# Performance work log

Measured on AMD Instinct MI355X. Metric: run time of the kernel, lower is better.

## Reference

```python
import jax, jax.numpy as jnp
from jax import lax
import numpy as np

LEAK = 0.95  # leaking_rate

SEQ, B, IN, H, OUT, L = 512, 32, 128, 2048, 128, 3


def setup_inputs() -> dict:
    key = jax.random.key(0)
    ks = jax.random.split(key, 12)
    in_scale = 1.0 / np.sqrt(IN)
    h_scale = 1.0 / np.sqrt(H)
    # spectral_radius=0.9: Gaussian NxN with std s has spectral radius ~ s*sqrt(N)
    rec_scale = 0.9 / np.sqrt(H)
    return {
        "input": jax.random.normal(ks[0], (SEQ, B, IN), jnp.float32),
        "w_ih0": jax.random.normal(ks[1], (H, IN), jnp.float32) * in_scale,
        "b_ih0": jax.random.normal(ks[2], (H,), jnp.float32) * 0.1,
        "w_hh0": jax.random.normal(ks[3], (H, H), jnp.float32) * rec_scale,
        "w_ih1": jax.random.normal(ks[4], (H, H), jnp.float32) * h_scale,
        "b_ih1": jax.random.normal(ks[5], (H,), jnp.float32) * 0.1,
        "w_hh1": jax.random.normal(ks[6], (H, H), jnp.float32) * rec_scale,
        "w_ih2": jax.random.normal(ks[7], (H, H), jnp.float32) * h_scale,
        "b_ih2": jax.random.normal(ks[8], (H,), jnp.float32) * 0.1,
        "w_hh2": jax.random.normal(ks[9], (H, H), jnp.float32) * rec_scale,
        "w_out": jax.random.normal(ks[10], (OUT, L * H), jnp.float32) * (1.0 / np.sqrt(L * H)),
        "b_out": jax.random.normal(ks[11], (OUT,), jnp.float32) * 0.1,
        "washout": 32,
    }


def reference(input, w_ih0, b_ih0, w_hh0, w_ih1, b_ih1, w_hh1,
              w_ih2, b_ih2, w_hh2, w_out, b_out, washout):
    a = jnp.asarray(LEAK, input.dtype)
    Bsz = input.shape[1]
    Hd = w_hh0.shape[0]

    def step(carry, x_t):
        h0, h1, h2 = carry
        # leaky-integrated tanh reservoir, layer-stacked (DeepESN)
        h0 = (1 - a) * h0 + a * jnp.tanh(x_t @ w_ih0.T + b_ih0 + h0 @ w_hh0.T)
        h1 = (1 - a) * h1 + a * jnp.tanh(h0 @ w_ih1.T + b_ih1 + h1 @ w_hh1.T)
        h2 = (1 - a) * h2 + a * jnp.tanh(h1 @ w_ih2.T + b_ih2 + h2 @ w_hh2.T)
        return (h0, h1, h2), jnp.concatenate([h0, h1, h2], axis=-1)

    init = tuple(jnp.zeros((Bsz, Hd), input.dtype) for _ in range(3))
    (h0, h1, h2), states = lax.scan(step, init, input)  # states: [S, B, L*H]
    states = states[washout:]                            # discard washout steps
    out = states @ w_out.T + b_out                       # [S-washout, B, OUT]
    hidden = jnp.stack([h0, h1, h2], axis=0)             # [L, B, H]
    return out, hidden
```

## Files before the change

### kernel.cpp

```cpp
#include <hip/hip_runtime.h>
#include <hip/hip_bf16.h>


typedef unsigned short u16;
typedef __attribute__((ext_vector_type(8))) __bf16 bf16x8;
typedef __attribute__((ext_vector_type(4))) float f32x4;

#define MFMA_AG(acc, a, w) \
  asm volatile("v_mfma_f32_16x16x32_bf16 %0, %1, %2, %0" : "+v"(acc) : "v"(a), "a"(w))

#define KC0 72
#define KC1 128
#define KCP 192
#define E0P (128*KC0*512)
#define E1P (128*KC1*512)
#define EPP (8*KCP*512)
#define CH 1024
#define S0 (68*CH)
#define S12 (64*CH)
#define NSLOT 8

static __device__ __forceinline__ float b2f(u16 u){ return __uint_as_float(((unsigned)u)<<16); }
static __device__ __forceinline__ u16 f2b(float f){ unsigned x=__float_as_uint(f); return (u16)((x + 0x7FFFu + ((x>>16)&1u))>>16); }
static __device__ __forceinline__ int frag_addr(int b, int j){
  int c=j>>5, ko=j&31, half=b>>4, lane=(b&15)|((ko>>3)<<4), e=ko&7;
  return ((c*2+half)*64+lane)*8+e;
}
static __device__ __forceinline__ bf16x8 asbf(f32x4 v){ union U{f32x4 f; bf16x8 b;} u; u.f=v; return u.b; }

static __device__ __forceinline__ f32x4 ld16_sc(const u16* p){
  f32x4 r;
  asm volatile("global_load_dwordx4 %0, %1, off sc0 sc1" : "=v"(r) : "v"(p));
  return r;
}
static __device__ __forceinline__ f32x4 ld16_pl(const float* p){
  f32x4 r;
  asm volatile("global_load_dwordx4 %0, %1, off" : "=v"(r) : "v"(p));
  return r;
}
static __device__ __forceinline__ void st_b128_sc(u16* p, f32x4 v){
  asm volatile("global_store_dwordx4 %0, %1, off sc0 sc1" :: "v"(p), "v"(v) : "memory");
}
static __device__ __forceinline__ void st_b32_sc(unsigned* p, unsigned v){
  asm volatile("global_store_dword %0, %1, off sc0 sc1" :: "v"(p), "v"(v) : "memory");
}
static __device__ __forceinline__ void drain(){
  asm volatile("s_waitcnt vmcnt(0)" ::: "memory");
}
#define WAITV(n) do{ asm volatile("s_waitcnt vmcnt(" #n ")" ::: "memory"); __builtin_amdgcn_sched_barrier(0); }while(0)

static __device__ __forceinline__ void poll4(int lane,
    const unsigned* a, unsigned ta,
    const unsigned* b, unsigned tb,
    const unsigned* c, unsigned tc, int nc,
    const unsigned* d, unsigned td)
{
  for(;;){
    unsigned va=0, vb=0, vc=0, vd=0;
    asm volatile("global_load_dword %0, %1, off sc0 sc1" : "=v"(va) : "v"(a+lane));
    if (b) asm volatile("global_load_dword %0, %1, off sc0 sc1" : "=v"(vb) : "v"(b+lane));
    if (c) asm volatile("global_load_dword %0, %1, off sc0 sc1" : "=v"(vc) : "v"(c+(lane<nc?lane:0)));
    if (d) asm volatile("global_load_dword %0, %1, off sc0 sc1" : "=v"(vd) : "v"(d+(lane<8?lane:0)));
    asm volatile("s_waitcnt vmcnt(0)" ::: "memory");
    __builtin_amdgcn_sched_barrier(0);
    bool ok = (va>=ta);
    if (b) ok &= (vb>=tb);
    if (c) ok &= (lane>=nc) || (vc>=tc);
    if (d) ok &= (lane>=8) || (vd>=td);
    if (__all(ok)) return;
    __builtin_amdgcn_s_sleep(1);
  }
}

__global__ __launch_bounds__(256) void k_pack(const float* __restrict__ wih0, const float* __restrict__ whh0,
    const float* __restrict__ wih1, const float* __restrict__ whh1,
    const float* __restrict__ wih2, const float* __restrict__ whh2,
    const float* __restrict__ wout,
    u16* __restrict__ p0, u16* __restrict__ p1, u16* __restrict__ p2, u16* __restrict__ po)
{
  const long SRC0 = 2048L*2176, SRC1 = 2048L*4096, SRCP = 128L*6144;
  const long total8 = (SRC0 + 2*SRC1 + SRCP) >> 3;
  for (long id = (long)blockIdx.x*blockDim.x + threadIdx.x; id < total8; id += (long)gridDim.x*blockDim.x){
    long r = id<<3; int KC, j, k; u16* dst;
    const float* sa; const float* sb; int split;
    if (r < SRC0){ KC=KC0; j=(int)(r/2176); k=(int)(r%2176); sa=wih0+(size_t)j*128; sb=whh0+(size_t)j*2048; split=128; dst=p0; }
    else if ((r -= SRC0) < SRC1){ KC=KC1; j=(int)(r/4096); k=(int)(r%4096); sa=wih1+(size_t)j*2048; sb=whh1+(size_t)j*2048; split=2048; dst=p1; }
    else if ((r -= SRC1) < SRC1){ KC=KC1; j=(int)(r/4096); k=(int)(r%4096); sa=wih2+(size_t)j*2048; sb=whh2+(size_t)j*2048; split=2048; dst=p2; }
    else { r -= SRC1; KC=KCP; j=(int)(r/6144); k=(int)(r%6144); sa=wout+(size_t)j*6144; sb=sa; split=6144; dst=po; }
    const float* src = (k<split) ? (sa + k) : (sb + (k - split));
    u16 tmp[8];
    #pragma unroll
    for (int e=0;e<8;e++) tmp[e] = f2b(src[e]);
    int jt=j>>4, jl=j&15, c=k>>5, ko=k&31, lane=((ko>>3)<<4)|jl;
    u16* dp = dst + (((size_t)jt*KC + c)*64 + lane)*8;
    *(f32x4*)dp = *(f32x4*)tmp;
  }
}

#define L12_ISS(s0, c0) \
  _Pragma("unroll") \
  for (int i=0;i<4;++i){ \
    sa[(s0)+i]=ld16_sc(apb + (size_t)((c0)+i)*CH); \
    sb[(s0)+i]=ld16_sc(apb + (size_t)((c0)+i)*CH + 512); \
  }
#define L12_MM(s0, c0) \
  _Pragma("unroll") \
  for (int i=0;i<4;++i){ \
    bf16x8 a0=asbf(sa[(s0)+i]), a1=asbf(sb[(s0)+i]); \
    MFMA_AG(acc00,a0,wreg[0][(c0)+i]); MFMA_AG(acc01,a1,wreg[0][(c0)+i]); \
    MFMA_AG(acc10,a0,wreg[1][(c0)+i]); MFMA_AG(acc11,a1,wreg[1][(c0)+i]); \
  }
#define PIN_ACC4() asm volatile("s_nop 1" : "+v"(acc00), "+v"(acc01), "+v"(acc10), "+v"(acc11))
#define FENCE_ACC4() asm volatile("s_nop 7\n\ts_nop 7" : "+v"(acc00), "+v"(acc01), "+v"(acc10), "+v"(acc11))

static __device__ __forceinline__ void run_l12(
    const u16* __restrict__ pW, const float* __restrict__ bias,
    const u16* __restrict__ A0slots, size_t a0stride, u16* OWN,
    unsigned* SEQup, unsigned* SEQown, unsigned* Sc, int nc, unsigned* Sd,
    int jt0, float (*red)[2][2][256], u16* ldsout)
{
  const int tid=threadIdx.x, w=tid>>6, ln=tid&63;
  bf16x8 wreg[2][16];
  #pragma unroll
  for (int u=0;u<2;u++)
    #pragma unroll
    for (int ci=0;ci<16;ci++)
      wreg[u][ci] = *(const bf16x8*)(pW + (((size_t)(jt0+u)*KC1 + (w*16+ci))*64 + ln)*8);

  const int h_=tid>>8, pos=tid&255, l_=pos>>2, i_=pos&3, col_=l_&15, row_=((l_>>4)<<2)+i_, b_=(h_<<4)+row_;
  const float bv0=bias[(jt0<<4)+col_], bv1=bias[((jt0+1)<<4)+col_];
  const int ko0=col_, ko1=16+col_;
  const int faw0=((h_*64)+((b_&15)|((ko0>>3)<<4)))*8+(ko0&7);
  const int faw1=((h_*64)+((b_&15)|((ko1>>3)<<4)))*8+(ko1&7);
  const int myc=jt0>>1, gidx=jt0>>1;

  if (tid<128) *(f32x4*)(ldsout+tid*8) = (f32x4){0,0,0,0};
  __syncthreads();

  for (int t=0;t<512;t++){
    if (tid<64){
      poll4(tid, SEQup,(unsigned)(t+1), SEQown,(unsigned)t,
            (t>=NSLOT)?Sc:nullptr,(unsigned)(t-7),nc,
            (t>=NSLOT)?Sd:nullptr,(unsigned)(t-7));
    }
    __syncthreads();
    const int cur=t&7, prv=(t+7)&7;
    const u16* a0base = (w<4) ? A0slots + (size_t)cur*a0stride + (size_t)(w*16)*CH
                              : OWN + (size_t)prv*S12 + (size_t)((w-4)*16)*CH;
    const u16* apb = a0base + (size_t)ln*8;
    f32x4 sa[8], sb[8];
    f32x4 acc00={0,0,0,0},acc01={0,0,0,0},acc10={0,0,0,0},acc11={0,0,0,0};
    PIN_ACC4();
    L12_ISS(0,0); L12_ISS(4,4);
    WAITV(8); L12_MM(0,0); L12_ISS(0,8);
    WAITV(8); L12_MM(4,4); L12_ISS(4,12);
    WAITV(8); L12_MM(0,8);
    WAITV(0); L12_MM(4,12);
    FENCE_ACC4();
    #pragma unroll
    for (int i=0;i<4;i++){
      red[w][0][0][(ln<<2)+i]=acc00[i]; red[w][0][1][(ln<<2)+i]=acc01[i];
      red[w][1][0][(ln<<2)+i]=acc10[i]; red[w][1][1][(ln<<2)+i]=acc11[i];
    }
    __syncthreads();
    {
      float v0=0.f, v1=0.f;
      #pragma unroll
      for (int ww=0;ww<8;ww++){ v0 += red[ww][0][h_][pos]; v1 += red[ww][1][h_][pos]; }
      float hp0 = b2f(ldsout[faw0]);
      float hp1 = b2f(ldsout[faw1]);
      ldsout[faw0] = f2b(0.05f*hp0 + 0.95f*tanhf(v0 + bv0));
      ldsout[faw1] = f2b(0.05f*hp1 + 0.95f*tanhf(v1 + bv1));
    }
    __syncthreads();
    if (tid<128){
      f32x4 vv = *(const f32x4*)(ldsout + tid*8);
      st_b128_sc(OWN + (size_t)cur*S12 + (size_t)myc*CH + tid*8, vv);
    }
    drain();
    __syncthreads();
    if (tid==0) st_b32_sc(SEQown+gidx, (unsigned)(t+1));
  }
}

#define X_ISSUE(ci) do{ \
    const float* q0 = xf + rr*128 + (ci)*32 + kg*8; \
    xs0[ci]=ld16_pl(q0); xs1[ci]=ld16_pl(q0+4); \
    xs2[ci]=ld16_pl(q0+2048); xs3[ci]=ld16_pl(q0+2052); \
  }while(0)
#define X_MFMA(ci) do{ \
    bf16x8 a0,a1; \
    _Pragma("unroll") \
    for (int e=0;e<4;e++){ a0[e]=(__bf16)xs0[ci][e]; a0[e+4]=(__bf16)xs1[ci][e]; \
                           a1[e]=(__bf16)xs2[ci][e]; a1[e+4]=(__bf16)xs3[ci][e]; } \
    asm volatile("s_nop 1" : "+v"(a0), "+v"(a1)); \
    MFMA_AG(acc00,a0,wreg[0][ci]); MFMA_AG(acc01,a1,wreg[0][ci]); \
    MFMA_AG(acc10,a0,wreg[1][ci]); MFMA_AG(acc11,a1,wreg[1][ci]); \
  }while(0)
#define LH_ISSUE(ci) do{ sa[ci]=ld16_sc(hbp + (size_t)(ci)*CH); sb[ci]=ld16_sc(hbp + (size_t)(ci)*CH + 512); }while(0)
#define LH_MFMA(ci) do{ \
    bf16x8 a0=asbf(sa[ci]), a1=asbf(sb[ci]); \
    MFMA_AG(acc00,a0,wreg[0][ci]); MFMA_AG(acc01,a1,wreg[0][ci]); \
    MFMA_AG(acc10,a0,wreg[1][ci]); MFMA_AG(acc11,a1,wreg[1][ci]); \
  }while(0)

static __device__ __forceinline__ void run_l0(
    const u16* __restrict__ pW, const float* __restrict__ bias, const float* __restrict__ input,
    u16* H0, unsigned* SEQ0, unsigned* SEQ1, unsigned* SEQ3,
    int jt0, float (*red)[2][2][256], u16* ldsout)
{
  const int tid=threadIdx.x, w=tid>>6, ln=tid&63, rr=ln&15, kg=ln>>4;
  bf16x8 wreg[2][9];
  #pragma unroll
  for (int u=0;u<2;u++)
    #pragma unroll
    for (int ci=0;ci<9;ci++)
      wreg[u][ci] = *(const bf16x8*)(pW + (((size_t)(jt0+u)*KC0 + (w*9+ci))*64 + ln)*8);

  const int h_=tid>>8, pos=tid&255, l_=pos>>2, i_=pos&3, col_=l_&15, row_=((l_>>4)<<2)+i_, b_=(h_<<4)+row_;
  const float bv0=bias[(jt0<<4)+col_], bv1=bias[((jt0+1)<<4)+col_];
  const int ko0=col_, ko1=16+col_;
  const int faw0=((h_*64)+((b_&15)|((ko0>>3)<<4)))*8+(ko0&7);
  const int faw1=((h_*64)+((b_&15)|((ko1>>3)<<4)))*8+(ko1&7);
  const int myc=jt0>>1, gidx=jt0>>1;

  if (tid<128) *(f32x4*)(ldsout+tid*8) = (f32x4){0,0,0,0};
  __syncthreads();

  for (int t=0;t<512;t++){
    if (tid<64){
      poll4(tid, SEQ0,(unsigned)t, (t>=NSLOT)?SEQ1:nullptr,(unsigned)(t-7),
            (t>=NSLOT)?SEQ3:nullptr,(unsigned)(t-7),8, nullptr,0u);
    }
    __syncthreads();
    const int cur=t&7, prv=(t+7)&7;
    const float* xf = input + (size_t)t*4096;
    const u16* h0prv = H0 + (size_t)prv*S0;
    f32x4 acc00={0,0,0,0},acc01={0,0,0,0},acc10={0,0,0,0},acc11={0,0,0,0};
    PIN_ACC4();
    if (w==0){
      f32x4 xs0[4],xs1[4],xs2[4],xs3[4], sa[9], sb[9];
      const u16* hbp = h0prv - (size_t)4*CH + (size_t)ln*8;
      X_ISSUE(0); X_ISSUE(1);
      X_ISSUE(2); X_ISSUE(3); WAITV(8); X_MFMA(0); X_MFMA(1);
      LH_ISSUE(4); LH_ISSUE(5); LH_ISSUE(6); LH_ISSUE(7); LH_ISSUE(8);
      WAITV(10); X_MFMA(2); X_MFMA(3);
      WAITV(0);
      LH_MFMA(4); LH_MFMA(5); LH_MFMA(6); LH_MFMA(7); LH_MFMA(8);
    } else {
      f32x4 sa[9], sb[9];
      const u16* hbp = h0prv + (size_t)(w*9-4)*CH + (size_t)ln*8;
      LH_ISSUE(0); LH_ISSUE(1); LH_ISSUE(2); LH_ISSUE(3);
      LH_ISSUE(4); LH_ISSUE(5); LH_ISSUE(6); LH_ISSUE(7);
      WAITV(8);  LH_MFMA(0); LH_MFMA(1); LH_MFMA(2); LH_MFMA(3);
      LH_ISSUE(8);
      WAITV(2);  LH_MFMA(4); LH_MFMA(5); LH_MFMA(6); LH_MFMA(7);
      WAITV(0);  LH_MFMA(8);
    }
    FENCE_ACC4();
    #pragma unroll
    for (int i=0;i<4;i++){
      red[w][0][0][(ln<<2)+i]=acc00[i]; red[w][0][1][(ln<<2)+i]=acc01[i];
      red[w][1][0][(ln<<2)+i]=acc10[i]; red[w][1][1][(ln<<2)+i]=acc11[i];
    }
    __syncthreads();
    {
      float v0=0.f, v1=0.f;
      #pragma unroll
      for (int ww=0;ww<8;ww++){ v0 += red[ww][0][h_][pos]; v1 += red[ww][1][h_][pos]; }
      float hp0 = b2f(ldsout[faw0]);
      float hp1 = b2f(ldsout[faw1]);
      ldsout[faw0] = f2b(0.05f*hp0 + 0.95f*tanhf(v0 + bv0));
      ldsout[faw1] = f2b(0.05f*hp1 + 0.95f*tanhf(v1 + bv1));
    }
    __syncthreads();
    if (tid<128){
      f32x4 vv = *(const f32x4*)(ldsout + tid*8);
      st_b128_sc(H0 + (size_t)cur*S0 + (size_t)myc*CH + tid*8, vv);
    }
    drain();
    __syncthreads();
    if (tid==0) st_b32_sc(SEQ0+gidx, (unsigned)(t+1));
  }
}

#define P_AP(kc_) ((kc_)<64 ? h0c+(size_t)(kc_)*CH : ((kc_)<128 ? h1c+(size_t)((kc_)-64)*CH : h2c+(size_t)((kc_)-128)*CH))
#define P_ISS(s0, c0) \
  _Pragma("unroll") \
  for (int i=0;i<6;++i){ \
    const u16* ap = P_AP(w*24+(c0)+i) + (size_t)ln*8; \
    sa[(s0)+i]=ld16_sc(ap); sb[(s0)+i]=ld16_sc(ap+512); \
  }
#define P_MM(s0, c0) \
  _Pragma("unroll") \
  for (int i=0;i<6;++i){ \
    bf16x8 a0=asbf(sa[(s0)+i]), a1=asbf(sb[(s0)+i]); \
    MFMA_AG(acc0,a0,wreg[(c0)+i]); MFMA_AG(acc1,a1,wreg[(c0)+i]); \
  }

static __device__ __forceinline__ void run_proj(
    const u16* __restrict__ pW, const float* __restrict__ bo,
    const u16* __restrict__ H0, const u16* __restrict__ H1, const u16* __restrict__ H2,
    float* __restrict__ out, const int* __restrict__ washp,
    unsigned* SEQ0, unsigned* SEQ1, unsigned* SEQ2, unsigned* SEQ3,
    int jt, float (*red)[2][2][256])
{
  const int tid=threadIdx.x, w=tid>>6, ln=tid&63;
  bf16x8 wreg[24];
  #pragma unroll
  for (int ci=0;ci<24;ci++)
    wreg[ci] = *(const bf16x8*)(pW + (((size_t)jt*KCP + (w*24+ci))*64 + ln)*8);
  const int wash = *washp;
  const int h_=tid>>8, pos=tid&255, l_=pos>>2, i_=pos&3, col_=l_&15, row_=((l_>>4)<<2)+i_, b_=(h_<<4)+row_;
  const float bvp = bo[(jt<<4)+col_];

  for (int t=0;t<512;t++){
    if (tid<64){
      poll4(tid, SEQ0,(unsigned)(t+1), SEQ1,(unsigned)(t+1), SEQ2,(unsigned)(t+1),64, nullptr,0u);
    }
    __syncthreads();
    const int cur=t&7;
    const u16* h0c = H0 + (size_t)cur*S0;
    const u16* h1c = H1 + (size_t)cur*S12;
    const u16* h2c = H2 + (size_t)cur*S12;
    f32x4 sa[12], sb[12];
    f32x4 acc0={0,0,0,0}, acc1={0,0,0,0};
    asm volatile("s_nop 1" : "+v"(acc0), "+v"(acc1));
    P_ISS(0,0); P_ISS(6,6);
    WAITV(12); P_MM(0,0);  P_ISS(0,12);
    WAITV(12); P_MM(6,6);  P_ISS(6,18);
    WAITV(12); P_MM(0,12);
    WAITV(0);  P_MM(6,18);
    asm volatile("s_nop 7\n\ts_nop 7" : "+v"(acc0), "+v"(acc1));
    #pragma unroll
    for (int i=0;i<4;i++){ red[w][0][0][(ln<<2)+i]=acc0[i]; red[w][0][1][(ln<<2)+i]=acc1[i]; }
    __syncthreads();
    if (tid==0) st_b32_sc(SEQ3+jt, (unsigned)(t+1));
    if (t >= wash){
      float v=0.f;
      #pragma unroll
      for (int ww=0;ww<8;ww++) v += red[ww][0][h_][pos];
      out[(((size_t)(t-wash))*32 + b_)*128 + (jt<<4)+col_] = v + bvp;
    }
    __syncthreads();
  }
  for (int q = jt*512 + tid; q < 196608; q += 4096){
    int l = q>>16, rem = q&65535, b = rem>>11, j = rem&2047;
    const u16* h = (l==0)? H0+(size_t)7*S0 : ((l==1)? H1+(size_t)7*S12 : H2+(size_t)7*S12);
    out[1966080 + q] = b2f(h[frag_addr(b,j)]);
  }
}

__global__ __launch_bounds__(512,2) void k_esn(
    const u16* __restrict__ p0, const u16* __restrict__ p1, const u16* __restrict__ p2, const u16* __restrict__ po,
    const float* __restrict__ b0, const float* __restrict__ b1, const float* __restrict__ b2, const float* __restrict__ bo,
    const float* __restrict__ input, const int* __restrict__ washp,
    u16* H0, u16* H1, u16* H2, unsigned* flags, float* out)
{
  __shared__ float red[8][2][2][256];
  __shared__ u16 ldsout[1024];
  const int bid = blockIdx.x;
  unsigned* SEQ0 = flags; unsigned* SEQ1 = flags+64; unsigned* SEQ2 = flags+128; unsigned* SEQ3 = flags+192;

  if (bid < 64)       run_l0 (p0, b0, input, H0, SEQ0, SEQ1, SEQ3, bid*2, red, ldsout);
  else if (bid < 128) run_l12(p1, b1, H0, S0,  H1, SEQ0, SEQ1, SEQ2, 64, SEQ3, (bid-64)*2, red, ldsout);
  else if (bid < 192) run_l12(p2, b2, H1, S12, H2, SEQ1, SEQ2, SEQ3, 8, nullptr, (bid-128)*2, red, ldsout);
  else                run_proj(po, bo, H0, H1, H2, out, washp, SEQ0, SEQ1, SEQ2, SEQ3, bid-192, red);
}

extern "C" void kernel_launch(void* const* d_in, const int* in_sizes, int n_in,
                              void* d_out, int out_size, void* d_ws, size_t ws_size,
                              hipStream_t stream)
{
  (void)in_sizes; (void)n_in; (void)out_size; (void)ws_size;
  const float* input=(const float*)d_in[0];
  const float* wih0=(const float*)d_in[1]; const float* bih0=(const float*)d_in[2];
  const float* whh0=(const float*)d_in[3];
  const float* wih1=(const float*)d_in[4]; const float* bih1=(const float*)d_in[5];
  const float* whh1=(const float*)d_in[6];
  const float* wih2=(const float*)d_in[7]; const float* bih2=(const float*)d_in[8];
  const float* whh2=(const float*)d_in[9];
  const float* wout=(const float*)d_in[10]; const float* bout=(const float*)d_in[11];
  const int* washp=(const int*)d_in[12];
  float* out=(float*)d_out;

  u16* p0=(u16*)d_ws;
  u16* p1=p0+E0P;
  u16* p2=p1+E1P;
  u16* po=p2+E1P;
  u16* H0=po+EPP;
  u16* H1=H0+(size_t)NSLOT*S0;
  u16* H2=H1+(size_t)NSLOT*S12;
  unsigned* flags=(unsigned*)(H2+(size_t)NSLOT*S12);
  size_t totbytes = ((char*)(flags+256)) - ((char*)d_ws);

  hipMemsetAsync(d_ws, 0, totbytes, stream);
  k_pack<<<dim3(2048),dim3(256),0,stream>>>(wih0,whh0,wih1,whh1,wih2,whh2,wout,p0,p1,p2,po);

  void* args[] = { (void*)&p0, (void*)&p1, (void*)&p2, (void*)&po,
                   (void*)&bih0, (void*)&bih1, (void*)&bih2, (void*)&bout,
                   (void*)&input, (void*)&washp,
                   (void*)&H0, (void*)&H1, (void*)&H2, (void*)&flags, (void*)&out };
  hipLaunchCooperativeKernel((const void*)k_esn, dim3(200), dim3(512), args, 0, stream);
}
```

Before: 4.912 ms.

## Use full per-timestep history buffers to drop slot-reuse backpressure polling

When the workspace is large enough, each timestep's hidden states get their own buffer (512 slots instead of an 8-slot ring). Producers therefore no longer poll downstream consumers before overwriting a slot, and the projection blocks stop publishing progress flags. Activation loads switch from sc0 sc1 to sc0 only, relying on an L2 invalidate at kernel start and coherent stores for packing and output. The cost is a much larger workspace footprint and more reliance on L2/device-level coherence semantics, and it falls back to the ring path when the workspace is too small.

```diff
diff --git a/kernel.cpp b/kernel.cpp
--- a/kernel.cpp
+++ b/kernel.cpp
@@ -28,9 +28,11 @@
 }
 static __device__ __forceinline__ bf16x8 asbf(f32x4 v){ union U{f32x4 f; bf16x8 b;} u; u.f=v; return u.b; }
 
-static __device__ __forceinline__ f32x4 ld16_sc(const u16* p){
+template<int BIG>
+static __device__ __forceinline__ f32x4 ld_act(const u16* p){
   f32x4 r;
-  asm volatile("global_load_dwordx4 %0, %1, off sc0 sc1" : "=v"(r) : "v"(p));
+  if constexpr (BIG) asm volatile("global_load_dwordx4 %0, %1, off sc0" : "=v"(r) : "v"(p));
+  else               asm volatile("global_load_dwordx4 %0, %1, off sc0 sc1" : "=v"(r) : "v"(p));
   return r;
 }
 static __device__ __forceinline__ f32x4 ld16_pl(const float* p){
@@ -41,11 +43,17 @@
 static __device__ __forceinline__ void st_b128_sc(u16* p, f32x4 v){
   asm volatile("global_store_dwordx4 %0, %1, off sc0 sc1" :: "v"(p), "v"(v) : "memory");
 }
+static __device__ __forceinline__ void st_f32_sc(float* p, float v){
+  asm volatile("global_store_dword %0, %1, off sc0 sc1" :: "v"(p), "v"(v) : "memory");
+}
 static __device__ __forceinline__ void st_b32_sc(unsigned* p, unsigned v){
   asm volatile("global_store_dword %0, %1, off sc0 sc1" :: "v"(p), "v"(v) : "memory");
 }
 static __device__ __forceinline__ void drain(){
   asm volatile("s_waitcnt vmcnt(0)" ::: "memory");
+}
+static __device__ __forceinline__ void l2_cleanse(){
+  asm volatile("buffer_inv sc1\n\ts_waitcnt vmcnt(0)" ::: "memory");
 }
 #define WAITV(n) do{ asm volatile("s_waitcnt vmcnt(" #n ")" ::: "memory"); __builtin_amdgcn_sched_barrier(0); }while(0)
 
@@ -93,15 +101,15 @@
     for (int e=0;e<8;e++) tmp[e] = f2b(src[e]);
     int jt=j>>4, jl=j&15, c=k>>5, ko=k&31, lane=((ko>>3)<<4)|jl;
     u16* dp = dst + (((size_t)jt*KC + c)*64 + lane)*8;
-    *(f32x4*)dp = *(f32x4*)tmp;
+    st_b128_sc(dp, *(f32x4*)tmp);
   }
 }
 
 #define L12_ISS(s0, c0) \
   _Pragma("unroll") \
   for (int i=0;i<4;++i){ \
-    sa[(s0)+i]=ld16_sc(apb + (size_t)((c0)+i)*CH); \
-    sb[(s0)+i]=ld16_sc(apb + (size_t)((c0)+i)*CH + 512); \
+    sa[(s0)+i]=ld_act<BIG>(apb + (size_t)((c0)+i)*CH); \
+    sb[(s0)+i]=ld_act<BIG>(apb + (size_t)((c0)+i)*CH + 512); \
   }
 #define L12_MM(s0, c0) \
   _Pragma("unroll") \
@@ -113,9 +121,10 @@
 #define PIN_ACC4() asm volatile("s_nop 1" : "+v"(acc00), "+v"(acc01), "+v"(acc10), "+v"(acc11))
 #define FENCE_ACC4() asm volatile("s_nop 7\n\ts_nop 7" : "+v"(acc00), "+v"(acc01), "+v"(acc10), "+v"(acc11))
 
+template<int BIG>
 static __device__ __forceinline__ void run_l12(
     const u16* __restrict__ pW, const float* __restrict__ bias,
-    const u16* __restrict__ A0slots, size_t a0stride, u16* OWN,
+    const u16* __restrict__ A0slots, size_t a0stride, u16* OWN, const u16* OWNZ,
     unsigned* SEQup, unsigned* SEQown, unsigned* Sc, int nc, unsigned* Sd,
     int jt0, float (*red)[2][2][256], u16* ldsout)
 {
@@ -139,14 +148,19 @@
 
   for (int t=0;t<512;t++){
     if (tid<64){
-      poll4(tid, SEQup,(unsigned)(t+1), SEQown,(unsigned)t,
-            (t>=NSLOT)?Sc:nullptr,(unsigned)(t-7),nc,
-            (t>=NSLOT)?Sd:nullptr,(unsigned)(t-7));
-    }
-    __syncthreads();
-    const int cur=t&7, prv=(t+7)&7;
-    const u16* a0base = (w<4) ? A0slots + (size_t)cur*a0stride + (size_t)(w*16)*CH
-                              : OWN + (size_t)prv*S12 + (size_t)((w-4)*16)*CH;
+      if constexpr (BIG)
+        poll4(tid, SEQup,(unsigned)(t+1), SEQown,(unsigned)t, nullptr,0u,0, nullptr,0u);
+      else
+        poll4(tid, SEQup,(unsigned)(t+1), SEQown,(unsigned)t,
+              (t>=NSLOT)?Sc:nullptr,(unsigned)(t-7),nc,
+              (t>=NSLOT)?Sd:nullptr,(unsigned)(t-7));
+    }
+    __syncthreads();
+    const u16* xa = A0slots + (size_t)(BIG ? t : (t&7))*a0stride;
+    const u16* xb = BIG ? (t==0 ? OWNZ : OWN + (size_t)(t-1)*S12)
+                        : OWN + (size_t)((t+7)&7)*S12;
+    u16* hc = OWN + (size_t)(BIG ? t : (t&7))*S12;
+    const u16* a0base = (w<4) ? xa + (size_t)(w*16)*CH : xb + (size_t)((w-4)*16)*CH;
     const u16* apb = a0base + (size_t)ln*8;
     f32x4 sa[8], sb[8];
     f32x4 acc00={0,0,0,0},acc01={0,0,0,0},acc10={0,0,0,0},acc11={0,0,0,0};
@@ -175,7 +189,7 @@
     __syncthreads();
     if (tid<128){
       f32x4 vv = *(const f32x4*)(ldsout + tid*8);
-      st_b128_sc(OWN + (size_t)cur*S12 + (size_t)myc*CH + tid*8, vv);
+      st_b128_sc(hc + (size_t)myc*CH + tid*8, vv);
     }
     drain();
     __syncthreads();
@@ -197,16 +211,17 @@
     MFMA_AG(acc00,a0,wreg[0][ci]); MFMA_AG(acc01,a1,wreg[0][ci]); \
     MFMA_AG(acc10,a0,wreg[1][ci]); MFMA_AG(acc11,a1,wreg[1][ci]); \
   }while(0)
-#define LH_ISSUE(ci) do{ sa[ci]=ld16_sc(hbp + (size_t)(ci)*CH); sb[ci]=ld16_sc(hbp + (size_t)(ci)*CH + 512); }while(0)
+#define LH_ISSUE(ci) do{ sa[ci]=ld_act<BIG>(hbp + (size_t)(ci)*CH); sb[ci]=ld_act<BIG>(hbp + (size_t)(ci)*CH + 512); }while(0)
 #define LH_MFMA(ci) do{ \
     bf16x8 a0=asbf(sa[ci]), a1=asbf(sb[ci]); \
     MFMA_AG(acc00,a0,wreg[0][ci]); MFMA_AG(acc01,a1,wreg[0][ci]); \
     MFMA_AG(acc10,a0,wreg[1][ci]); MFMA_AG(acc11,a1,wreg[1][ci]); \
   }while(0)
 
+template<int BIG>
 static __device__ __forceinline__ void run_l0(
     const u16* __restrict__ pW, const float* __restrict__ bias, const float* __restrict__ input,
-    u16* H0, unsigned* SEQ0, unsigned* SEQ1, unsigned* SEQ3,
+    u16* H0, const u16* HZ0, unsigned* SEQ0, unsigned* SEQ1, unsigned* SEQ3,
     int jt0, float (*red)[2][2][256], u16* ldsout)
 {
   const int tid=threadIdx.x, w=tid>>6, ln=tid&63, rr=ln&15, kg=ln>>4;
@@ -229,13 +244,17 @@
 
   for (int t=0;t<512;t++){
     if (tid<64){
-      poll4(tid, SEQ0,(unsigned)t, (t>=NSLOT)?SEQ1:nullptr,(unsigned)(t-7),
-            (t>=NSLOT)?SEQ3:nullptr,(unsigned)(t-7),8, nullptr,0u);
-    }
-    __syncthreads();
-    const int cur=t&7, prv=(t+7)&7;
+      if constexpr (BIG)
+        poll4(tid, SEQ0,(unsigned)t, nullptr,0u, nullptr,0u,0, nullptr,0u);
+      else
+        poll4(tid, SEQ0,(unsigned)t, (t>=NSLOT)?SEQ1:nullptr,(unsigned)(t-7),
+              (t>=NSLOT)?SEQ3:nullptr,(unsigned)(t-7),8, nullptr,0u);
+    }
+    __syncthreads();
     const float* xf = input + (size_t)t*4096;
-    const u16* h0prv = H0 + (size_t)prv*S0;
+    const u16* h0prv = BIG ? (t==0 ? HZ0 : H0 + (size_t)(t-1)*S0)
+                           : H0 + (size_t)((t+7)&7)*S0;
+    u16* hc = H0 + (size_t)(BIG ? t : (t&7))*S0;
     f32x4 acc00={0,0,0,0},acc01={0,0,0,0},acc10={0,0,0,0},acc11={0,0,0,0};
     PIN_ACC4();
     if (w==0){
@@ -276,7 +295,7 @@
     __syncthreads();
     if (tid<128){
       f32x4 vv = *(const f32x4*)(ldsout + tid*8);
-      st_b128_sc(H0 + (size_t)cur*S0 + (size_t)myc*CH + tid*8, vv);
+      st_b128_sc(hc + (size_t)myc*CH + tid*8, vv);
     }
     drain();
     __syncthreads();
@@ -289,7 +308,7 @@
   _Pragma("unroll") \
   for (int i=0;i<6;++i){ \
     const u16* ap = P_AP(w*24+(c0)+i) + (size_t)ln*8; \
-    sa[(s0)+i]=ld16_sc(ap); sb[(s0)+i]=ld16_sc(ap+512); \
+    sa[(s0)+i]=ld_act<BIG>(ap); sb[(s0)+i]=ld_act<BIG>(ap+512); \
   }
 #define P_MM(s0, c0) \
   _Pragma("unroll") \
@@ -298,6 +317,7 @@
     MFMA_AG(acc0,a0,wreg[(c0)+i]); MFMA_AG(acc1,a1,wreg[(c0)+i]); \
   }
 
+template<int BIG>
 static __device__ __forceinline__ void run_proj(
     const u16* __restrict__ pW, const float* __restrict__ bo,
     const u16* __restrict__ H0, const u16* __restrict__ H1, const u16* __restrict__ H2,
@@ -319,10 +339,10 @@
       poll4(tid, SEQ0,(unsigned)(t+1), SEQ1,(unsigned)(t+1), SEQ2,(unsigned)(t+1),64, nullptr,0u);
     }
     __syncthreads();
-    const int cur=t&7;
-    const u16* h0c = H0 + (size_t)cur*S0;
-    const u16* h1c = H1 + (size_t)cur*S12;
-    const u16* h2c = H2 + (size_t)cur*S12;
+    const size_t sl = BIG ? (size_t)t : (size_t)(t&7);
+    const u16* h0c = H0 + sl*S0;
+    const u16* h1c = H1 + sl*S12;
+    const u16* h2c = H2 + sl*S12;
     f32x4 sa[12], sb[12];
     f32x4 acc0={0,0,0,0}, acc1={0,0,0,0};
     asm volatile("s_nop 1" : "+v"(acc0), "+v"(acc1));
@@ -335,44 +355,63 @@
     #pragma unroll
     for (int i=0;i<4;i++){ red[w][0][0][(ln<<2)+i]=acc0[i]; red[w][0][1][(ln<<2)+i]=acc1[i]; }
     __syncthreads();
-    if (tid==0) st_b32_sc(SEQ3+jt, (unsigned)(t+1));
+    if constexpr (!BIG){ if (tid==0) st_b32_sc(SEQ3+jt, (unsigned)(t+1)); }
     if (t >= wash){
       float v=0.f;
       #pragma unroll
       for (int ww=0;ww<8;ww++) v += red[ww][0][h_][pos];
-      out[(((size_t)(t-wash))*32 + b_)*128 + (jt<<4)+col_] = v + bvp;
-    }
-    __syncthreads();
-  }
-  for (int q = jt*512 + tid; q < 196608; q += 4096){
-    int l = q>>16, rem = q&65535, b = rem>>11, j = rem&2047;
-    const u16* h = (l==0)? H0+(size_t)7*S0 : ((l==1)? H1+(size_t)7*S12 : H2+(size_t)7*S12);
-    out[1966080 + q] = b2f(h[frag_addr(b,j)]);
-  }
-}
-
+      st_f32_sc(&out[(((size_t)(t-wash))*32 + b_)*128 + (jt<<4)+col_], v + bvp);
+    }
+    __syncthreads();
+  }
+  {
+    const size_t sl = BIG ? (size_t)511 : (size_t)7;
+    const u16* H0s = H0 + sl*S0;
+    const u16* H1s = H1 + sl*S12;
+    const u16* H2s = H2 + sl*S12;
+    for (int q = jt*512 + tid; q < 196608; q += 4096){
+      int l = q>>16, rem = q&65535, b = rem>>11, j = rem&2047;
+      const u16* h = (l==0)? H0s : ((l==1)? H1s : H2s);
+      unsigned tmp;
+      if constexpr (BIG)
+        asm volatile("global_load_ushort %0, %1, off sc0" : "=v"(tmp) : "v"(h+frag_addr(b,j)));
+      else
+        asm volatile("global_load_ushort %0, %1, off sc0 sc1" : "=v"(tmp) : "v"(h+frag_addr(b,j)));
+      asm volatile("s_waitcnt vmcnt(0)" ::: "memory");
+      st_f32_sc(&out[1966080 + q], b2f((u16)tmp));
+    }
+  }
+}
+
+template<int BIG>
 __global__ __launch_bounds__(512,2) void k_esn(
     const u16* __restrict__ p0, const u16* __restrict__ p1, const u16* __restrict__ p2, const u16* __restrict__ po,
     const float* __restrict__ b0, const float* __restrict__ b1, const float* __restrict__ b2, const float* __restrict__ bo,
     const float* __restrict__ input, const int* __restrict__ washp,
-    u16* H0, u16* H1, u16* H2, unsigned* flags, float* out)
+    u16* H0, u16* H1, u16* H2, const u16* HZ0, const u16* HZ12,
+    unsigned* flags, float* out)
 {
   __shared__ float red[8][2][2][256];
   __shared__ u16 ldsout[1024];
-  const int bid = blockIdx.x;
+  const int bid = blockIdx.x, tid = threadIdx.x;
   unsigned* SEQ0 = flags; unsigned* SEQ1 = flags+64; unsigned* SEQ2 = flags+128; unsigned* SEQ3 = flags+192;
 
-  if (bid < 64)       run_l0 (p0, b0, input, H0, SEQ0, SEQ1, SEQ3, bid*2, red, ldsout);
-  else if (bid < 128) run_l12(p1, b1, H0, S0,  H1, SEQ0, SEQ1, SEQ2, 64, SEQ3, (bid-64)*2, red, ldsout);
-  else if (bid < 192) run_l12(p2, b2, H1, S12, H2, SEQ1, SEQ2, SEQ3, 8, nullptr, (bid-128)*2, red, ldsout);
-  else                run_proj(po, bo, H0, H1, H2, out, washp, SEQ0, SEQ1, SEQ2, SEQ3, bid-192, red);
+  if constexpr (BIG){
+    if (tid < 64) l2_cleanse();
+    __syncthreads();
+  }
+
+  if (bid < 64)       run_l0<BIG> (p0, b0, input, H0, HZ0, SEQ0, SEQ1, SEQ3, bid*2, red, ldsout);
+  else if (bid < 128) run_l12<BIG>(p1, b1, H0, S0,  H1, HZ12, SEQ0, SEQ1, SEQ2, 64, SEQ3, (bid-64)*2, red, ldsout);
+  else if (bid < 192) run_l12<BIG>(p2, b2, H1, S12, H2, HZ12, SEQ1, SEQ2, SEQ3, 8, nullptr, (bid-128)*2, red, ldsout);
+  else                run_proj<BIG>(po, bo, H0, H1, H2, out, washp, SEQ0, SEQ1, SEQ2, SEQ3, bid-192, red);
 }
 
 extern "C" void kernel_launch(void* const* d_in, const int* in_sizes, int n_in,
                               void* d_out, int out_size, void* d_ws, size_t ws_size,
                               hipStream_t stream)
 {
-  (void)in_sizes; (void)n_in; (void)out_size; (void)ws_size;
+  (void)in_sizes; (void)n_in; (void)out_size;
   const float* input=(const float*)d_in[0];
   const float* wih0=(const float*)d_in[1]; const float* bih0=(const float*)d_in[2];
   const float* whh0=(const float*)d_in[3];
@@ -388,18 +427,31 @@
   u16* p1=p0+E0P;
   u16* p2=p1+E1P;
   u16* po=p2+E1P;
-  u16* H0=po+EPP;
-  u16* H1=H0+(size_t)NSLOT*S0;
-  u16* H2=H1+(size_t)NSLOT*S12;
-  unsigned* flags=(unsigned*)(H2+(size_t)NSLOT*S12);
-  size_t totbytes = ((char*)(flags+256)) - ((char*)d_ws);
-
-  hipMemsetAsync(d_ws, 0, totbytes, stream);
+  unsigned* flags=(unsigned*)(po+EPP);
+  u16* HZ0=(u16*)(flags+256);
+  u16* HZ12=HZ0+S0;
+  u16* H0=HZ12+S12;
+
+  size_t bigH0=(size_t)512*S0, bigH12=(size_t)512*S12;
+  size_t need_big = ((size_t)(H0 - p0) + bigH0 + 2*bigH12) * sizeof(u16);
+  int big = (ws_size >= need_big) ? 1 : 0;
+
+  size_t nslot = big ? 512 : NSLOT;
+  u16* H1 = H0 + nslot*S0;
+  u16* H2 = H1 + nslot*S12;
+
+  size_t clr = ((size_t)(H0 - p0))*sizeof(u16);
+  if (!big) clr = ((size_t)(H2 + nslot*S12 - p0))*sizeof(u16);
+  hipMemsetAsync(d_ws, 0, clr, stream);
   k_pack<<<dim3(2048),dim3(256),0,stream>>>(wih0,whh0,wih1,whh1,wih2,whh2,wout,p0,p1,p2,po);
 
   void* args[] = { (void*)&p0, (void*)&p1, (void*)&p2, (void*)&po,
                    (void*)&bih0, (void*)&bih1, (void*)&bih2, (void*)&bout,
                    (void*)&input, (void*)&washp,
-                   (void*)&H0, (void*)&H1, (void*)&H2, (void*)&flags, (void*)&out };
-  hipLaunchCooperativeKernel((const void*)k_esn, dim3(200), dim3(512), args, 0, stream);
-}
+                   (void*)&H0, (void*)&H1, (void*)&H2, (void*)&HZ0, (void*)&HZ12,
+                   (void*)&flags, (void*)&out };
+  if (big)
+    hipLaunchCooperativeKernel((const void*)k_esn<1>, dim3(200), dim3(512), args, 0, stream);
+  else
+    hipLaunchCooperativeKernel((const void*)k_esn<0>, dim3(200), dim3(512), args, 0, stream);
+}
```

Result: slower. 6.113 ms (+24.5%).
